# Kernel optimization log

Hardware: AMD Instinct MI355X
Metric: run time of the kernel (lower is better)

Reference implementation:

```python
import jax, jax.numpy as jnp
import numpy as np

N = 10000        # nodes
E = 320000       # edges
IN = 256         # input_dim
D = 64           # output_dim per head
H = 4            # num_heads
ED = 32          # edge_dim
T = 8            # num_etypes
SLOPE = 0.2      # leaky relu negative slope


def setup_inputs() -> dict:
    key = jax.random.key(0)
    ks = jax.random.split(key, 12)
    s = 0.05
    feat = jax.random.normal(ks[0], (N, IN), jnp.float32)
    edge_weight = jax.random.uniform(ks[1], (E,), jnp.float32)
    row = jax.random.randint(ks[2], (E,), 0, N, jnp.int32)
    col = jax.random.randint(ks[3], (E,), 0, N, jnp.int32)
    etype_idxs = jax.random.randint(ks[4], (E,), 0, T, jnp.int32)
    W = jax.random.normal(ks[5], (IN, D * H), jnp.float32) * s
    edge_emb_table = jax.random.normal(ks[6], (T, ED), jnp.float32) * s
    W_r = jax.random.normal(ks[7], (T, ED, ED * H), jnp.float32) * s
    a_l = jax.random.normal(ks[8], (H, D), jnp.float32) * s
    a_r = jax.random.normal(ks[9], (H, D), jnp.float32) * s
    a_e = jax.random.normal(ks[10], (H, ED), jnp.float32) * s
    W_res = jax.random.normal(ks[11], (IN, D * H), jnp.float32) * s
    b_res = jnp.zeros((D * H,), jnp.float32)
    return dict(feat=feat, edge_weight=edge_weight, row=row, col=col,
                etype_idxs=etype_idxs, W=W, edge_emb_table=edge_emb_table,
                W_r=W_r, a_l=a_l, a_r=a_r, a_e=a_e, W_res=W_res, b_res=b_res)


def reference(feat, edge_weight, row, col, etype_idxs, W, edge_emb_table,
              W_r, a_l, a_r, a_e, W_res, b_res):
    # node projection: [N, H, D]
    emb = jnp.nan_to_num(feat @ W).reshape(N, H, D)
    # typed linear on edge-type embeddings: only T distinct outputs, gather per edge
    type_out = jnp.einsum('ti,tio->to', edge_emb_table, W_r).reshape(T, H, ED)
    edge_e = type_out[etype_idxs]                      # [E, H, ED]
    # attention logits
    hl = jnp.einsum('nhd,hd->nh', emb, a_l)            # [N, H]
    hr = jnp.einsum('nhd,hd->nh', emb, a_r)            # [N, H]
    he = jnp.einsum('ehd,hd->eh', edge_e, a_e)         # [E, H]
    att = jax.nn.sigmoid(jax.nn.leaky_relu(hl[row] + hr[col] + he, SLOPE))
    att = att * edge_weight[:, None]                   # [E, H]
    # u_mul_e + sum scatter: src=row, dst=col
    msg = emb[row] * att[:, :, None]                   # [E, H, D]
    agg = jax.ops.segment_sum(msg, col, num_segments=N)  # [N, H, D]
    # original permutes to [N, D, H] before flattening
    out = jnp.transpose(agg, (0, 2, 1)).reshape(N, D * H)
    out = out + feat @ W_res + b_res                   # residual
    return jax.nn.elu(out)
```

## Files before the change

kernel.cpp:

```cpp
#include <hip/hip_runtime.h>
#include <hip/hip_bf16.h>
#include <math.h>

#define N_NODES 10000
#define MPAD 10112
#define N_EDGES 320000
#define IN_DIM 256
#define NH 4
#define EDIM 32
#define NT 8
#define SLOPE 0.2f
#define CAP 96

#define WTW (512 * 256)
#define GB (MPAD / 32)
#define EBT 512
#define EB ((N_EDGES + EBT - 1) / EBT)

typedef __attribute__((ext_vector_type(8))) short short8b;
typedef __attribute__((ext_vector_type(4))) float f32x4;

__device__ __forceinline__ float bf2f(ushort u) {
  return __uint_as_float(((unsigned)u) << 16);
}
__device__ __forceinline__ ushort f2bf(float f) {
  __hip_bfloat16 h = __float2bfloat16(f);
  return *(ushort*)&h;
}
__device__ __forceinline__ unsigned pk2(float a, float b) {
  return (unsigned)f2bf(a) | ((unsigned)f2bf(b) << 16);
}

__global__ void prep_kernel(const float* __restrict__ W,
                            const float* __restrict__ W_res,
                            const float* __restrict__ table,
                            const float* __restrict__ W_r,
                            const float* __restrict__ a_e,
                            ushort* __restrict__ Wtb,
                            float* __restrict__ he_type,
                            int* __restrict__ cnt) {
  int i = blockIdx.x * 256 + threadIdx.x;
  if (i < WTW) {
    int c = i >> 8, k = i & 255;
    float v = (c < 256) ? W[k * 256 + ((c & 3) * 64 + (c >> 2))]
                        : W_res[k * 256 + (c - 256)];
    Wtb[c * 256 + k] = f2bf(v);
  } else if (i < WTW + 1024) {
    int t2 = i - WTW;
    int t = t2 >> 7, h = (t2 >> 5) & 3, d = t2 & 31;
    float acc = 0.f;
    for (int q = 0; q < EDIM; ++q)
      acc += table[t * EDIM + q] * W_r[(t * EDIM + q) * (EDIM * NH) + h * EDIM + d];
    acc *= a_e[h * EDIM + d];
#pragma unroll
    for (int o = 16; o; o >>= 1) acc += __shfl_xor(acc, o, 32);
    if (d == 0) he_type[t * NH + h] = acc;
  } else {
    int z = i - WTW - 1024;
    if (z <= N_NODES) cnt[z] = 0;
  }
}

__global__ __launch_bounds__(512) void gemm_bucket_kernel(
    const float* __restrict__ feat, const ushort* __restrict__ Wtb,
    const float* __restrict__ b_res,
    const float* __restrict__ a_l, const float* __restrict__ a_r,
    ushort* __restrict__ emb_t, ushort* __restrict__ resb,
    float* __restrict__ hl, float* __restrict__ hr,
    const int* __restrict__ row, const int* __restrict__ colv,
    const int* __restrict__ et, const float* __restrict__ ew,
    int* cnt, uint2* __restrict__ slots) {
  __shared__ ushort As[32 * 256];
  const int tid = threadIdx.x;

  if (blockIdx.x >= GB) {
    int e = (blockIdx.x - GB) * EBT + tid;
    if (e < N_EDGES) {
      int r = row[e], c = colv[e], t = et[e];
      float w = ew[e];
      uint2 slot;
      slot.x = ((unsigned)t << 16) | (unsigned)r;
      slot.y = __float_as_uint(w);
      int s = atomicAdd(&cnt[c], 1);
      if (s < CAP) slots[(size_t)c * CAP + s] = slot;
    }
    return;
  }

  const int rowbase = blockIdx.x * 32;

#pragma unroll
  for (int i = 0; i < 2; ++i) {
    int c = tid + i * 512;
    int rowl = c >> 5, slot = c & 31;
    int gr = rowbase + rowl;
    uint4 pk = make_uint4(0, 0, 0, 0);
    if (gr < N_NODES) {
      float4 x = *(const float4*)&feat[(size_t)gr * 256 + slot * 8];
      float4 y = *(const float4*)&feat[(size_t)gr * 256 + slot * 8 + 4];
      pk.x = pk2(x.x, x.y); pk.y = pk2(x.z, x.w);
      pk.z = pk2(y.x, y.y); pk.w = pk2(y.z, y.w);
    }
    int idx = rowl * 256 + (((slot * 16) ^ ((rowl & 7) << 4)) >> 1);
    *(uint4*)&As[idx] = pk;
  }
  __syncthreads();

  const int wave = tid >> 6, lane = tid & 63;
  const int col0 = wave * 64;
  const int lr = lane & 15;
  const int lkq = lane >> 4;
  f32x4 acc[4][2] = {};
  const ushort* Bb = Wtb + (size_t)(col0 + lr) * 256 + lkq * 8;

#pragma unroll
  for (int ks = 0; ks < 8; ++ks) {
    short8b a[2], b[4];
#pragma unroll
    for (int m = 0; m < 2; ++m) {
      int rowl = m * 16 + lr;
      int kb = ks * 64 + lkq * 16;
      int idx = rowl * 256 + ((kb ^ ((rowl & 7) << 4)) >> 1);
      a[m] = *(const short8b*)&As[idx];
    }
#pragma unroll
    for (int n = 0; n < 4; ++n)
      b[n] = *(const short8b*)(Bb + (size_t)(n * 16) * 256 + ks * 32);
#pragma unroll
    for (int n = 0; n < 4; ++n)
#pragma unroll
      for (int m = 0; m < 2; ++m)
        acc[n][m] = __builtin_amdgcn_mfma_f32_16x16x32_bf16(b[n], a[m], acc[n][m], 0, 0, 0);
  }

  float pl[2][4] = {{0.f}}, pr[2][4] = {{0.f}};
  if (col0 < 256) {
#pragma unroll
    for (int m = 0; m < 2; ++m) {
      int r = rowbase + m * 16 + lr;
      if (r < N_NODES) {
#pragma unroll
        for (int n = 0; n < 4; ++n) {
          int d = (col0 >> 2) + n * 4 + lkq;
          ushort4 pk4;
          pk4.x = f2bf(acc[n][m][0]); pk4.y = f2bf(acc[n][m][1]);
          pk4.z = f2bf(acc[n][m][2]); pk4.w = f2bf(acc[n][m][3]);
          *(ushort4*)&emb_t[((size_t)r * 64 + d) * 4] = pk4;
        }
      }
    }
#pragma unroll
    for (int n = 0; n < 4; ++n) {
      int d = (col0 >> 2) + n * 4 + lkq;
#pragma unroll
      for (int h = 0; h < 4; ++h) {
        float alv = a_l[h * 64 + d];
        float arv = a_r[h * 64 + d];
#pragma unroll
        for (int m = 0; m < 2; ++m) {
          pl[m][h] = fmaf(acc[n][m][h], alv, pl[m][h]);
          pr[m][h] = fmaf(acc[n][m][h], arv, pr[m][h]);
        }
      }
    }
#pragma unroll
    for (int m = 0; m < 2; ++m)
#pragma unroll
      for (int h = 0; h < 4; ++h) {
        pl[m][h] += __shfl_xor(pl[m][h], 16);
        pl[m][h] += __shfl_xor(pl[m][h], 32);
        pr[m][h] += __shfl_xor(pr[m][h], 16);
        pr[m][h] += __shfl_xor(pr[m][h], 32);
      }
  } else {
#pragma unroll
    for (int m = 0; m < 2; ++m) {
      int r = rowbase + m * 16 + lr;
      if (r < N_NODES) {
#pragma unroll
        for (int n = 0; n < 4; ++n) {
          int c = (col0 - 256) + n * 16 + lkq * 4;
          float4 br = *(const float4*)&b_res[c];
          ushort4 pk4;
          pk4.x = f2bf(acc[n][m][0] + br.x); pk4.y = f2bf(acc[n][m][1] + br.y);
          pk4.z = f2bf(acc[n][m][2] + br.z); pk4.w = f2bf(acc[n][m][3] + br.w);
          *(ushort4*)&resb[(size_t)r * 256 + c] = pk4;
        }
      }
    }
  }

  float* PL = (float*)As;
  float* PR = PL + 512;
  __syncthreads();
  if (col0 < 256 && lkq == 0) {
#pragma unroll
    for (int m = 0; m < 2; ++m)
#pragma unroll
      for (int h = 0; h < 4; ++h) {
        PL[(wave * 32 + m * 16 + lr) * 4 + h] = pl[m][h];
        PR[(wave * 32 + m * 16 + lr) * 4 + h] = pr[m][h];
      }
  }
  __syncthreads();
  if (tid < 64) {
    int rl = tid >> 1, sel = tid & 1;
    const float* P = sel ? PR : PL;
    float4 v;
    v.x = P[rl * 4 + 0] + P[128 + rl * 4 + 0] + P[256 + rl * 4 + 0] + P[384 + rl * 4 + 0];
    v.y = P[rl * 4 + 1] + P[128 + rl * 4 + 1] + P[256 + rl * 4 + 1] + P[384 + rl * 4 + 1];
    v.z = P[rl * 4 + 2] + P[128 + rl * 4 + 2] + P[256 + rl * 4 + 2] + P[384 + rl * 4 + 2];
    v.w = P[rl * 4 + 3] + P[128 + rl * 4 + 3] + P[256 + rl * 4 + 3] + P[384 + rl * 4 + 3];
    int r = rowbase + rl;
    if (r < N_NODES) *(float4*)&(sel ? hr : hl)[r * 4] = v;
  }
}

__global__ __launch_bounds__(256) void agg_kernel(
    const int* __restrict__ cnt, const uint2* __restrict__ slots,
    const float* __restrict__ hl, const float* __restrict__ hr,
    const float* __restrict__ he_type,
    const ushort* __restrict__ emb_t, const ushort* __restrict__ resb,
    float* __restrict__ out) {
  __shared__ uint4 meta[4 * CAP];
  const int wv = threadIdx.x >> 6;
  const int lane = threadIdx.x & 63;
  const int nu = __builtin_amdgcn_readfirstlane(blockIdx.x * 4 + wv);
  const int cn = min(cnt[nu], CAP);

  {
    float4 R = *(const float4*)&hr[nu * 4];
    for (int j = lane; j < cn; j += 64) {
      uint2 s = slots[(size_t)nu * CAP + j];
      int src = s.x & 0xffff, t = s.x >> 16;
      float w = __uint_as_float(s.y);
      float4 L = *(const float4*)&hl[src * 4];
      float4 He = *(const float4*)&he_type[t * 4];
      float x[4] = {L.x + R.x + He.x, L.y + R.y + He.y,
                    L.z + R.z + He.z, L.w + R.w + He.w};
      float a[4];
#pragma unroll
      for (int h = 0; h < 4; ++h) {
        float v = x[h];
        v = v >= 0.f ? v : SLOPE * v;
        a[h] = w / (1.f + __expf(-v));
      }
      uint4 m;
      m.x = pk2(a[0], a[1]);
      m.y = pk2(a[2], a[3]);
      m.z = (unsigned)src;
      m.w = 0;
      meta[wv * CAP + j] = m;
    }
  }
  __syncthreads();

  float acc0 = 0.f, acc1 = 0.f, acc2 = 0.f, acc3 = 0.f;
  const uint4* mb = &meta[wv * CAP];

#define AGG_FMA(V, WA, WB)                                      \
  acc0 = fmaf(bf2f((V).x), __uint_as_float((WA) << 16), acc0);  \
  acc1 = fmaf(bf2f((V).y), __uint_as_float((WA) & 0xffff0000u), acc1); \
  acc2 = fmaf(bf2f((V).z), __uint_as_float((WB) << 16), acc2);  \
  acc3 = fmaf(bf2f((V).w), __uint_as_float((WB) & 0xffff0000u), acc3);

  const int j4 = cn & ~3;
#pragma unroll 2
  for (int j = 0; j < j4; j += 4) {
    uint4 m0 = mb[j], m1 = mb[j + 1], m2 = mb[j + 2], m3 = mb[j + 3];
    ushort4 v0 = *(const ushort4*)&emb_t[((size_t)m0.z * 64 + lane) * 4];
    ushort4 v1 = *(const ushort4*)&emb_t[((size_t)m1.z * 64 + lane) * 4];
    ushort4 v2 = *(const ushort4*)&emb_t[((size_t)m2.z * 64 + lane) * 4];
    ushort4 v3 = *(const ushort4*)&emb_t[((size_t)m3.z * 64 + lane) * 4];
    AGG_FMA(v0, m0.x, m0.y)
    AGG_FMA(v1, m1.x, m1.y)
    AGG_FMA(v2, m2.x, m2.y)
    AGG_FMA(v3, m3.x, m3.y)
  }
  for (int j = j4; j < cn; ++j) {
    uint4 m0 = mb[j];
    ushort4 v0 = *(const ushort4*)&emb_t[((size_t)m0.z * 64 + lane) * 4];
    AGG_FMA(v0, m0.x, m0.y)
  }
#undef AGG_FMA

  ushort4 r4 = *(const ushort4*)&resb[((size_t)nu * 64 + lane) * 4];
  float v0 = acc0 + bf2f(r4.x), v1 = acc1 + bf2f(r4.y);
  float v2 = acc2 + bf2f(r4.z), v3 = acc3 + bf2f(r4.w);
  float4 o;
  o.x = v0 > 0.f ? v0 : expm1f(v0);
  o.y = v1 > 0.f ? v1 : expm1f(v1);
  o.z = v2 > 0.f ? v2 : expm1f(v2);
  o.w = v3 > 0.f ? v3 : expm1f(v3);
  *(float4*)&out[((size_t)nu * 64 + lane) * 4] = o;
}

extern "C" void kernel_launch(void* const* d_in, const int* in_sizes, int n_in,
                              void* d_out, int out_size, void* d_ws, size_t ws_size,
                              hipStream_t stream) {
  const float* feat = (const float*)d_in[0];
  const float* ew = (const float*)d_in[1];
  const int* row = (const int*)d_in[2];
  const int* col = (const int*)d_in[3];
  const int* etype = (const int*)d_in[4];
  const float* W = (const float*)d_in[5];
  const float* table = (const float*)d_in[6];
  const float* W_r = (const float*)d_in[7];
  const float* a_l = (const float*)d_in[8];
  const float* a_r = (const float*)d_in[9];
  const float* a_e = (const float*)d_in[10];
  const float* W_res = (const float*)d_in[11];
  const float* b_res = (const float*)d_in[12];
  float* out = (float*)d_out;

  char* w = (char*)d_ws;
  auto alloc = [&](size_t bytes) {
    char* pp = w;
    w += (bytes + 255) & ~(size_t)255;
    return pp;
  };
  ushort* Wtb = (ushort*)alloc((size_t)512 * 256 * 2);
  ushort* emb_t = (ushort*)alloc((size_t)N_NODES * 256 * 2);
  ushort* resb = (ushort*)alloc((size_t)N_NODES * 256 * 2);
  uint2* slots = (uint2*)alloc((size_t)N_NODES * CAP * 8);
  float* hl = (float*)alloc((size_t)N_NODES * NH * 4);
  float* hr = (float*)alloc((size_t)N_NODES * NH * 4);
  float* he_type = (float*)alloc(NT * NH * 4);
  int* cnt = (int*)alloc((size_t)(N_NODES + 1) * 4);

  const int PREP_BLOCKS = WTW / 256 + 4 + (N_NODES + 256) / 256;
  prep_kernel<<<PREP_BLOCKS, 256, 0, stream>>>(W, W_res, table, W_r, a_e,
                                               Wtb, he_type, cnt);
  gemm_bucket_kernel<<<GB + EB, 512, 0, stream>>>(
      feat, Wtb, b_res, a_l, a_r, emb_t, resb, hl, hr,
      row, col, etype, ew, cnt, slots);
  agg_kernel<<<N_NODES / 4, 256, 0, stream>>>(cnt, slots, hl, hr, he_type,
                                              emb_t, resb, out);
}
```

Baseline: 57.73 us.

## Halve GEMM row tile and split each node's edge aggregation across two waves

The GEMM block tile drops from 32 to 16 rows, which doubles the number of GEMM blocks and halves per-block LDS and accumulator use. The aggregation kernel now gives each destination node two waves. Each wave computes attention and gathers over half the edge list, then the partial sums are combined through shared memory before the residual and ELU. This is meant to raise parallelism and latency hiding for the gather-bound aggregation, at the cost of twice as many blocks, an extra reduction, and less B-operand reuse per block in the GEMM.

```diff
diff --git a/kernel.cpp b/kernel.cpp
--- a/kernel.cpp
+++ b/kernel.cpp
@@ -13,7 +13,7 @@
 #define CAP 96
 
 #define WTW (512 * 256)
-#define GB (MPAD / 32)
+#define GB (MPAD / 16)
 #define EBT 512
 #define EB ((N_EDGES + EBT - 1) / EBT)
 
@@ -70,7 +70,7 @@
     const int* __restrict__ row, const int* __restrict__ colv,
     const int* __restrict__ et, const float* __restrict__ ew,
     int* cnt, uint2* __restrict__ slots) {
-  __shared__ ushort As[32 * 256];
+  __shared__ ushort As[16 * 256];
   const int tid = threadIdx.x;
 
   if (blockIdx.x >= GB) {
@@ -87,12 +87,10 @@
     return;
   }
 
-  const int rowbase = blockIdx.x * 32;
-
-#pragma unroll
-  for (int i = 0; i < 2; ++i) {
-    int c = tid + i * 512;
-    int rowl = c >> 5, slot = c & 31;
+  const int rowbase = blockIdx.x * 16;
+
+  {
+    int rowl = tid >> 5, slot = tid & 31;
     int gr = rowbase + rowl;
     uint4 pk = make_uint4(0, 0, 0, 0);
     if (gr < N_NODES) {
@@ -110,43 +108,36 @@
   const int col0 = wave * 64;
   const int lr = lane & 15;
   const int lkq = lane >> 4;
-  f32x4 acc[4][2] = {};
+  f32x4 acc[4] = {};
   const ushort* Bb = Wtb + (size_t)(col0 + lr) * 256 + lkq * 8;
 
 #pragma unroll
   for (int ks = 0; ks < 8; ++ks) {
-    short8b a[2], b[4];
-#pragma unroll
-    for (int m = 0; m < 2; ++m) {
-      int rowl = m * 16 + lr;
+    short8b a, b[4];
+    {
       int kb = ks * 64 + lkq * 16;
-      int idx = rowl * 256 + ((kb ^ ((rowl & 7) << 4)) >> 1);
-      a[m] = *(const short8b*)&As[idx];
+      int idx = lr * 256 + ((kb ^ ((lr & 7) << 4)) >> 1);
+      a = *(const short8b*)&As[idx];
     }
 #pragma unroll
     for (int n = 0; n < 4; ++n)
       b[n] = *(const short8b*)(Bb + (size_t)(n * 16) * 256 + ks * 32);
 #pragma unroll
     for (int n = 0; n < 4; ++n)
-#pragma unroll
-      for (int m = 0; m < 2; ++m)
-        acc[n][m] = __builtin_amdgcn_mfma_f32_16x16x32_bf16(b[n], a[m], acc[n][m], 0, 0, 0);
-  }
-
-  float pl[2][4] = {{0.f}}, pr[2][4] = {{0.f}};
+      acc[n] = __builtin_amdgcn_mfma_f32_16x16x32_bf16(b[n], a, acc[n], 0, 0, 0);
+  }
+
+  float pl[4] = {0.f, 0.f, 0.f, 0.f}, pr[4] = {0.f, 0.f, 0.f, 0.f};
+  const int r = rowbase + lr;
   if (col0 < 256) {
-#pragma unroll
-    for (int m = 0; m < 2; ++m) {
-      int r = rowbase + m * 16 + lr;
-      if (r < N_NODES) {
-#pragma unroll
-        for (int n = 0; n < 4; ++n) {
-          int d = (col0 >> 2) + n * 4 + lkq;
-          ushort4 pk4;
-          pk4.x = f2bf(acc[n][m][0]); pk4.y = f2bf(acc[n][m][1]);
-          pk4.z = f2bf(acc[n][m][2]); pk4.w = f2bf(acc[n][m][3]);
-          *(ushort4*)&emb_t[((size_t)r * 64 + d) * 4] = pk4;
-        }
+    if (r < N_NODES) {
+#pragma unroll
+      for (int n = 0; n < 4; ++n) {
+        int d = (col0 >> 2) + n * 4 + lkq;
+        ushort4 pk4;
+        pk4.x = f2bf(acc[n][0]); pk4.y = f2bf(acc[n][1]);
+        pk4.z = f2bf(acc[n][2]); pk4.w = f2bf(acc[n][3]);
+        *(ushort4*)&emb_t[((size_t)r * 64 + d) * 4] = pk4;
       }
     }
 #pragma unroll
@@ -154,65 +145,52 @@
       int d = (col0 >> 2) + n * 4 + lkq;
 #pragma unroll
       for (int h = 0; h < 4; ++h) {
-        float alv = a_l[h * 64 + d];
-        float arv = a_r[h * 64 + d];
-#pragma unroll
-        for (int m = 0; m < 2; ++m) {
-          pl[m][h] = fmaf(acc[n][m][h], alv, pl[m][h]);
-          pr[m][h] = fmaf(acc[n][m][h], arv, pr[m][h]);
-        }
+        pl[h] = fmaf(acc[n][h], a_l[h * 64 + d], pl[h]);
+        pr[h] = fmaf(acc[n][h], a_r[h * 64 + d], pr[h]);
       }
     }
 #pragma unroll
-    for (int m = 0; m < 2; ++m)
-#pragma unroll
-      for (int h = 0; h < 4; ++h) {
-        pl[m][h] += __shfl_xor(pl[m][h], 16);
-        pl[m][h] += __shfl_xor(pl[m][h], 32);
-        pr[m][h] += __shfl_xor(pr[m][h], 16);
-        pr[m][h] += __shfl_xor(pr[m][h], 32);
+    for (int h = 0; h < 4; ++h) {
+      pl[h] += __shfl_xor(pl[h], 16);
+      pl[h] += __shfl_xor(pl[h], 32);
+      pr[h] += __shfl_xor(pr[h], 16);
+      pr[h] += __shfl_xor(pr[h], 32);
+    }
+  } else {
+    if (r < N_NODES) {
+#pragma unroll
+      for (int n = 0; n < 4; ++n) {
+        int c = (col0 - 256) + n * 16 + lkq * 4;
+        float4 br = *(const float4*)&b_res[c];
+        ushort4 pk4;
+        pk4.x = f2bf(acc[n][0] + br.x); pk4.y = f2bf(acc[n][1] + br.y);
+        pk4.z = f2bf(acc[n][2] + br.z); pk4.w = f2bf(acc[n][3] + br.w);
+        *(ushort4*)&resb[(size_t)r * 256 + c] = pk4;
       }
-  } else {
-#pragma unroll
-    for (int m = 0; m < 2; ++m) {
-      int r = rowbase + m * 16 + lr;
-      if (r < N_NODES) {
-#pragma unroll
-        for (int n = 0; n < 4; ++n) {
-          int c = (col0 - 256) + n * 16 + lkq * 4;
-          float4 br = *(const float4*)&b_res[c];
-          ushort4 pk4;
-          pk4.x = f2bf(acc[n][m][0] + br.x); pk4.y = f2bf(acc[n][m][1] + br.y);
-          pk4.z = f2bf(acc[n][m][2] + br.z); pk4.w = f2bf(acc[n][m][3] + br.w);
-          *(ushort4*)&resb[(size_t)r * 256 + c] = pk4;
-        }
-      }
     }
   }
 
   float* PL = (float*)As;
-  float* PR = PL + 512;
+  float* PR = PL + 256;
   __syncthreads();
   if (col0 < 256 && lkq == 0) {
 #pragma unroll
-    for (int m = 0; m < 2; ++m)
-#pragma unroll
-      for (int h = 0; h < 4; ++h) {
-        PL[(wave * 32 + m * 16 + lr) * 4 + h] = pl[m][h];
-        PR[(wave * 32 + m * 16 + lr) * 4 + h] = pr[m][h];
-      }
+    for (int h = 0; h < 4; ++h) {
+      PL[(wave * 16 + lr) * 4 + h] = pl[h];
+      PR[(wave * 16 + lr) * 4 + h] = pr[h];
+    }
   }
   __syncthreads();
-  if (tid < 64) {
+  if (tid < 32) {
     int rl = tid >> 1, sel = tid & 1;
     const float* P = sel ? PR : PL;
     float4 v;
-    v.x = P[rl * 4 + 0] + P[128 + rl * 4 + 0] + P[256 + rl * 4 + 0] + P[384 + rl * 4 + 0];
-    v.y = P[rl * 4 + 1] + P[128 + rl * 4 + 1] + P[256 + rl * 4 + 1] + P[384 + rl * 4 + 1];
-    v.z = P[rl * 4 + 2] + P[128 + rl * 4 + 2] + P[256 + rl * 4 + 2] + P[384 + rl * 4 + 2];
-    v.w = P[rl * 4 + 3] + P[128 + rl * 4 + 3] + P[256 + rl * 4 + 3] + P[384 + rl * 4 + 3];
-    int r = rowbase + rl;
-    if (r < N_NODES) *(float4*)&(sel ? hr : hl)[r * 4] = v;
+    v.x = P[rl * 4 + 0] + P[64 + rl * 4 + 0] + P[128 + rl * 4 + 0] + P[192 + rl * 4 + 0];
+    v.y = P[rl * 4 + 1] + P[64 + rl * 4 + 1] + P[128 + rl * 4 + 1] + P[192 + rl * 4 + 1];
+    v.z = P[rl * 4 + 2] + P[64 + rl * 4 + 2] + P[128 + rl * 4 + 2] + P[192 + rl * 4 + 2];
+    v.w = P[rl * 4 + 3] + P[64 + rl * 4 + 3] + P[128 + rl * 4 + 3] + P[192 + rl * 4 + 3];
+    int gr = rowbase + rl;
+    if (gr < N_NODES) *(float4*)&(sel ? hr : hl)[gr * 4] = v;
   }
 }
 
@@ -222,15 +200,21 @@
     const float* __restrict__ he_type,
     const ushort* __restrict__ emb_t, const ushort* __restrict__ resb,
     float* __restrict__ out) {
-  __shared__ uint4 meta[4 * CAP];
+  __shared__ uint4 meta[2 * CAP];
+  __shared__ float accs[2][64][4];
   const int wv = threadIdx.x >> 6;
   const int lane = threadIdx.x & 63;
-  const int nu = __builtin_amdgcn_readfirstlane(blockIdx.x * 4 + wv);
+  const int nb = wv >> 1;
+  const int half = wv & 1;
+  const int nu = __builtin_amdgcn_readfirstlane(blockIdx.x * 2 + nb);
   const int cn = min(cnt[nu], CAP);
+  const int c0 = (cn >> 1) & ~3;
+  const int jlo = half ? c0 : 0;
+  const int jhi = half ? cn : c0;
 
   {
     float4 R = *(const float4*)&hr[nu * 4];
-    for (int j = lane; j < cn; j += 64) {
+    for (int j = jlo + lane; j < jhi; j += 64) {
       uint2 s = slots[(size_t)nu * CAP + j];
       int src = s.x & 0xffff, t = s.x >> 16;
       float w = __uint_as_float(s.y);
@@ -250,13 +234,12 @@
       m.y = pk2(a[2], a[3]);
       m.z = (unsigned)src;
       m.w = 0;
-      meta[wv * CAP + j] = m;
-    }
-  }
-  __syncthreads();
+      meta[nb * CAP + j] = m;
+    }
+  }
 
   float acc0 = 0.f, acc1 = 0.f, acc2 = 0.f, acc3 = 0.f;
-  const uint4* mb = &meta[wv * CAP];
+  const uint4* mb = &meta[nb * CAP];
 
 #define AGG_FMA(V, WA, WB)                                      \
   acc0 = fmaf(bf2f((V).x), __uint_as_float((WA) << 16), acc0);  \
@@ -264,9 +247,9 @@
   acc2 = fmaf(bf2f((V).z), __uint_as_float((WB) << 16), acc2);  \
   acc3 = fmaf(bf2f((V).w), __uint_as_float((WB) & 0xffff0000u), acc3);
 
-  const int j4 = cn & ~3;
+  const int jq = jlo + ((jhi - jlo) & ~3);
 #pragma unroll 2
-  for (int j = 0; j < j4; j += 4) {
+  for (int j = jlo; j < jq; j += 4) {
     uint4 m0 = mb[j], m1 = mb[j + 1], m2 = mb[j + 2], m3 = mb[j + 3];
     ushort4 v0 = *(const ushort4*)&emb_t[((size_t)m0.z * 64 + lane) * 4];
     ushort4 v1 = *(const ushort4*)&emb_t[((size_t)m1.z * 64 + lane) * 4];
@@ -277,22 +260,31 @@
     AGG_FMA(v2, m2.x, m2.y)
     AGG_FMA(v3, m3.x, m3.y)
   }
-  for (int j = j4; j < cn; ++j) {
+  for (int j = jq; j < jhi; ++j) {
     uint4 m0 = mb[j];
     ushort4 v0 = *(const ushort4*)&emb_t[((size_t)m0.z * 64 + lane) * 4];
     AGG_FMA(v0, m0.x, m0.y)
   }
 #undef AGG_FMA
 
-  ushort4 r4 = *(const ushort4*)&resb[((size_t)nu * 64 + lane) * 4];
-  float v0 = acc0 + bf2f(r4.x), v1 = acc1 + bf2f(r4.y);
-  float v2 = acc2 + bf2f(r4.z), v3 = acc3 + bf2f(r4.w);
-  float4 o;
-  o.x = v0 > 0.f ? v0 : expm1f(v0);
-  o.y = v1 > 0.f ? v1 : expm1f(v1);
-  o.z = v2 > 0.f ? v2 : expm1f(v2);
-  o.w = v3 > 0.f ? v3 : expm1f(v3);
-  *(float4*)&out[((size_t)nu * 64 + lane) * 4] = o;
+  if (half == 1) {
+    accs[nb][lane][0] = acc0; accs[nb][lane][1] = acc1;
+    accs[nb][lane][2] = acc2; accs[nb][lane][3] = acc3;
+  }
+  __syncthreads();
+  if (half == 0) {
+    acc0 += accs[nb][lane][0]; acc1 += accs[nb][lane][1];
+    acc2 += accs[nb][lane][2]; acc3 += accs[nb][lane][3];
+    ushort4 r4 = *(const ushort4*)&resb[((size_t)nu * 64 + lane) * 4];
+    float v0 = acc0 + bf2f(r4.x), v1 = acc1 + bf2f(r4.y);
+    float v2 = acc2 + bf2f(r4.z), v3 = acc3 + bf2f(r4.w);
+    float4 o;
+    o.x = v0 > 0.f ? v0 : expm1f(v0);
+    o.y = v1 > 0.f ? v1 : expm1f(v1);
+    o.z = v2 > 0.f ? v2 : expm1f(v2);
+    o.w = v3 > 0.f ? v3 : expm1f(v3);
+    *(float4*)&out[((size_t)nu * 64 + lane) * 4] = o;
+  }
 }
 
 extern "C" void kernel_launch(void* const* d_in, const int* in_sizes, int n_in,
@@ -334,6 +326,6 @@
   gemm_bucket_kernel<<<GB + EB, 512, 0, stream>>>(
       feat, Wtb, b_res, a_l, a_r, emb_t, resb, hl, hr,
       row, col, etype, ew, cnt, slots);
-  agg_kernel<<<N_NODES / 4, 256, 0, stream>>>(cnt, slots, hl, hr, he_type,
+  agg_kernel<<<N_NODES / 2, 256, 0, stream>>>(cnt, slots, hl, hr, he_type,
                                               emb_t, resb, out);
 }
```

Result: slower. 66.30 us (+14.8%).
